# Kernel tuning notes

Measured on AMD Instinct MI355X. Metric: run time of the kernel, lower is better.

The kernel has to match this reference:

```python
import math
import jax, jax.numpy as jnp
import numpy as np

HEADS = 9
EMBED = 32
TEMPERATURE = 3000.0

def _conv1x1(x, W, b):
    # x: [B,C,H,W], W: [O,C], b: [O]  (1x1 conv == channel matmul)
    return jnp.einsum('bchw,oc->bohw', x, W) + b[None, :, None, None]

def setup_inputs() -> dict:
    key = jax.random.key(0)
    ks = jax.random.split(key, 14)
    B, H, W = 2, 64, 64
    h2, w2 = 32, 32
    hd = HEADS * EMBED  # 288
    s = 0.1
    return {
        'second_frame': jax.random.normal(ks[0], (B, 3, H, W), jnp.float32),
        'first_frame_aligned': jax.random.normal(ks[1], (B, 3, H, W), jnp.float32),
        'second_frame_feat': jax.random.normal(ks[2], (B, 4, h2, w2), jnp.float32),
        'first_frame_feat_aligned': jax.random.normal(ks[3], (B, 4, h2, w2), jnp.float32),
        'Wq': jax.random.normal(ks[4], (hd, 3), jnp.float32) * s,
        'bq': jax.random.normal(ks[5], (hd,), jnp.float32) * s,
        'Wk': jax.random.normal(ks[6], (hd, 3), jnp.float32) * s,
        'bk': jax.random.normal(ks[7], (hd,), jnp.float32) * s,
        'Wv': jax.random.normal(ks[8], (hd, 4), jnp.float32) * s,
        'bv': jax.random.normal(ks[9], (hd,), jnp.float32) * s,
        'Wp': jax.random.normal(ks[10], (4, hd), jnp.float32) * s,
        'bp': jax.random.normal(ks[11], (4,), jnp.float32) * s,
        'Wt': jax.random.normal(ks[12], (1, EMBED), jnp.float32) * s,
        'bt': jax.random.normal(ks[13], (1,), jnp.float32) * s,
    }

def reference(second_frame, first_frame_aligned, second_frame_feat,
              first_frame_feat_aligned, Wq, bq, Wk, bk, Wv, bv, Wp, bp, Wt, bt):
    B, _, H, W = second_frame.shape
    HW = H * W
    # bilinear upsample of aligned features to (H, W); half-pixel centers == align_corners=False
    feat_up = jax.image.resize(first_frame_feat_aligned,
                               (B, first_frame_feat_aligned.shape[1], H, W),
                               method='linear', antialias=False)
    Q = _conv1x1(second_frame, Wq, bq).reshape(B, HEADS, EMBED, HW)
    K = _conv1x1(first_frame_aligned, Wk, bk).reshape(B, HEADS, EMBED, HW)
    V = _conv1x1(feat_up, Wv, bv).reshape(B, HEADS, EMBED, HW)
    Qn = jnp.transpose(Q, (0, 1, 3, 2))                      # [B,h,HW,d]
    sim = jnp.einsum('bhnd,bhdm->bhnm', Qn, K) / math.sqrt(EMBED)  # [B,h,HW,HW]
    # learned per-query threshold from Q
    t = jnp.einsum('bhnd,od->bhno', Qn, Wt) + bt             # [B,h,HW,1]
    attn = jax.nn.relu((sim - t) / TEMPERATURE)              # no row normalization
    out = jnp.einsum('bhnm,bhdm->bhnd', attn, V)             # [B,h,HW,d]
    out = jnp.transpose(out, (0, 1, 3, 2)).reshape(B, HEADS * EMBED, H, W)
    out_feat = _conv1x1(out, Wp, bp)                         # [B,4,H,W]
    h2, w2 = second_frame_feat.shape[-2:]
    out_feat_down = jax.image.resize(out_feat, (B, out_feat.shape[1], h2, w2),
                                     method='linear', antialias=False)
    final_feat = second_frame_feat + out_feat_down
    return final_feat, out_feat_down
```

## Files before the change

### kernel.cpp

```cpp
#include <hip/hip_runtime.h>
#include <hip/hip_bf16.h>
#include <cstddef>

#define NHEADS 9
#define D 32
#define SQ 4096
#define ZSPLIT 8
#define MBLK (SQ / ZSPLIT)
#define CHUNKS (MBLK / 64)
#define KROW 40
#define VROW 72

typedef __attribute__((ext_vector_type(8))) short bf16x8;
typedef __attribute__((ext_vector_type(4))) short bf16x4;
typedef __attribute__((ext_vector_type(4))) float f32x4;

__device__ __forceinline__ unsigned int f2bf(float f) {
    unsigned int u = __float_as_uint(f);
    u += 0x7fffu + ((u >> 16) & 1u);
    return u >> 16;
}

__device__ __forceinline__ unsigned int trunc_pk(float lo, float hi) {
    return __builtin_amdgcn_perm(__float_as_uint(hi), __float_as_uint(lo),
                                 0x07060302u);
}

__device__ __forceinline__ bf16x8 relu_pack8(f32x4 s1, f32x4 s2) {
    const f32x4 zz = {0.f, 0.f, 0.f, 0.f};
    f32x4 a = __builtin_elementwise_max(s1, zz);
    f32x4 b = __builtin_elementwise_max(s2, zz);
    union { unsigned int u[4]; bf16x8 v; } P;
    P.u[0] = trunc_pk(a[0], a[1]);
    P.u[1] = trunc_pk(a[2], a[3]);
    P.u[2] = trunc_pk(b[0], b[1]);
    P.u[3] = trunc_pk(b[2], b[3]);
    return P.v;
}

__global__ __launch_bounds__(256) void prep_kernel(
    const float* __restrict__ x2, const float* __restrict__ x1,
    const float* __restrict__ feat1,
    const float* __restrict__ Wq, const float* __restrict__ bq,
    const float* __restrict__ Wk, const float* __restrict__ bk,
    const float* __restrict__ Wv, const float* __restrict__ bv,
    const float* __restrict__ Wt, const float* __restrict__ bt,
    unsigned short* __restrict__ Qb, unsigned short* __restrict__ Kb,
    unsigned short* __restrict__ Vt, float* __restrict__ tbuf,
    float* __restrict__ of)
{
    __shared__ unsigned short Vls[32 * 66];

    const int tid = threadIdx.x;
    int idx = blockIdx.x * blockDim.x + tid;
    if (idx < 2 * 4 * SQ) of[idx] = 0.0f;
    int g  = idx & 3;
    int nl = tid >> 2;
    int n  = (idx >> 2) & (SQ - 1);
    int bh = idx >> 14;
    int h  = bh % NHEADS;
    int b  = bh / NHEADS;

    float xs0 = x2[((size_t)b * 3 + 0) * SQ + n];
    float xs1 = x2[((size_t)b * 3 + 1) * SQ + n];
    float xs2 = x2[((size_t)b * 3 + 2) * SQ + n];
    float ys0 = x1[((size_t)b * 3 + 0) * SQ + n];
    float ys1 = x1[((size_t)b * 3 + 1) * SQ + n];
    float ys2 = x1[((size_t)b * 3 + 2) * SQ + n];

    int yy = n >> 6, xx = n & 63;
    int jy = yy >> 1, jx = xx >> 1;
    int j0, j1, i0, i1; float wy0, wy1, wx0, wx1;
    if (yy & 1) { j0 = jy; j1 = (jy < 31) ? jy + 1 : 31; wy0 = 0.75f; wy1 = 0.25f; }
    else        { j0 = (jy > 0) ? jy - 1 : 0; j1 = jy;   wy0 = 0.25f; wy1 = 0.75f; }
    if (xx & 1) { i0 = jx; i1 = (jx < 31) ? jx + 1 : 31; wx0 = 0.75f; wx1 = 0.25f; }
    else        { i0 = (jx > 0) ? jx - 1 : 0; i1 = jx;   wx0 = 0.25f; wx1 = 0.75f; }

    float fu[4];
#pragma unroll
    for (int c = 0; c < 4; ++c) {
        const float* f = feat1 + ((size_t)b * 4 + c) * 1024;
        fu[c] = wy0 * (wx0 * f[j0 * 32 + i0] + wx1 * f[j0 * 32 + i1]) +
                wy1 * (wx0 * f[j1 * 32 + i0] + wx1 * f[j1 * 32 + i1]);
    }

    const int d0 = g * 8;
    unsigned int qp[4], kp[4];
    float tpart = 0.0f;
#pragma unroll
    for (int j = 0; j < 8; ++j) {
        int d = d0 + j, hd = h * D + d;
        float q = bq[hd] + Wq[hd * 3] * xs0 + Wq[hd * 3 + 1] * xs1 + Wq[hd * 3 + 2] * xs2;
        float k = bk[hd] + Wk[hd * 3] * ys0 + Wk[hd * 3 + 1] * ys1 + Wk[hd * 3 + 2] * ys2;
        float v = bv[hd] + Wv[hd * 4] * fu[0] + Wv[hd * 4 + 1] * fu[1] +
                  Wv[hd * 4 + 2] * fu[2] + Wv[hd * 4 + 3] * fu[3];
        tpart += q * Wt[d];
        unsigned int qb_ = f2bf(q), kb_ = f2bf(k);
        if (j & 1) { qp[j >> 1] |= qb_ << 16; kp[j >> 1] |= kb_ << 16; }
        else       { qp[j >> 1]  = qb_;       kp[j >> 1]  = kb_; }
        Vls[d * 66 + nl] = (unsigned short)f2bf(v);
    }
    tpart += __shfl_xor(tpart, 1);
    tpart += __shfl_xor(tpart, 2);
    if (g == 0) tbuf[(size_t)bh * SQ + n] = tpart + bt[0];

    size_t base = ((size_t)bh * SQ + n) * D + d0;
    *(uint4*)(Qb + base) = make_uint4(qp[0], qp[1], qp[2], qp[3]);
    *(uint4*)(Kb + base) = make_uint4(kp[0], kp[1], kp[2], kp[3]);

    __syncthreads();
    {
        int r  = tid >> 3;
        int c4 = tid & 7;
        int n0 = (blockIdx.x & 63) * 64;
        unsigned int w0 = *(const unsigned int*)&Vls[r * 66 + c4 * 4];
        unsigned int w1 = *(const unsigned int*)&Vls[r * 66 + c4 * 4 + 2];
        *(uint2*)(Vt + ((size_t)bh * D + r) * SQ + n0 + c4 * 4) = make_uint2(w0, w1);
    }
}

__global__ __launch_bounds__(256, 4) void attn_kernel(
    const unsigned short* __restrict__ Qb,
    const unsigned short* __restrict__ Kb,
    const unsigned short* __restrict__ Vt,
    const float* __restrict__ tbuf,
    const float* __restrict__ Wp,
    float* __restrict__ of)
{
    __shared__ __align__(16) unsigned short Ks[64 * KROW];
    __shared__ __align__(16) unsigned short Vs[32 * VROW];

    const int bh   = blockIdx.y;
    const int h    = bh % NHEADS;
    const int b    = bh / NHEADS;
    const int n0   = blockIdx.x * 256;
    const int mc0  = blockIdx.z * MBLK;
    const int tid  = threadIdx.x;
    const int wave = tid >> 6;
    const int lane = tid & 63;
    const int l15  = lane & 15;
    const int quad = lane >> 4;

    const int nw = n0 + wave * 64;

    const unsigned short* qbase = Qb + ((size_t)bh * SQ + nw + l15) * D + quad * 8;
    bf16x8 qfA = *(const bf16x8*)(qbase);
    bf16x8 qfB = *(const bf16x8*)(qbase + 16 * D);
    bf16x8 qfC = *(const bf16x8*)(qbase + 32 * D);
    bf16x8 qfD = *(const bf16x8*)(qbase + 48 * D);

    const float SQRT32 = 5.656854249492381f;
    const float* tb = tbuf + (size_t)bh * SQ + nw + l15;
    float TA = tb[0]  * SQRT32;
    float TB = tb[16] * SQRT32;
    float TC = tb[32] * SQRT32;
    float TD = tb[48] * SQRT32;
    const f32x4 ciA = {-TA, -TA, -TA, -TA};
    const f32x4 ciB = {-TB, -TB, -TB, -TB};
    const f32x4 ciC = {-TC, -TC, -TC, -TC};
    const f32x4 ciD = {-TD, -TD, -TD, -TD};

    const uint4* Kg4 = (const uint4*)(Kb + (size_t)bh * SQ * D);
    const uint4* Vg4 = (const uint4*)(Vt + (size_t)bh * D * SQ);

    const int krow = tid >> 2;
    const int kcol = (tid & 3) * 8;
    const int kslot = (krow & 32) + 4 * ((krow >> 3) & 3) + (krow & 3) + ((krow & 4) << 2);
    unsigned short* kdst = Ks + kslot * KROW + kcol;
    const int vd = tid >> 3;
    const int vm = (tid & 7) * 8;
    unsigned short* vdst = Vs + vd * VROW + vm;
    const int vgbase = vd * (SQ / 8) + (mc0 >> 3) + (tid & 7);

    f32x4 accAl = {0.f,0.f,0.f,0.f}, accAh = {0.f,0.f,0.f,0.f};
    f32x4 accBl = {0.f,0.f,0.f,0.f}, accBh = {0.f,0.f,0.f,0.f};
    f32x4 accCl = {0.f,0.f,0.f,0.f}, accCh = {0.f,0.f,0.f,0.f};
    f32x4 accDl = {0.f,0.f,0.f,0.f}, accDh = {0.f,0.f,0.f,0.f};

    uint4 kreg = Kg4[(size_t)mc0 * 4 + tid];
    uint4 vreg = Vg4[vgbase];

    for (int c = 0; c < CHUNKS; ++c) {
        __syncthreads();
        *(uint4*)kdst = kreg;
        *(uint4*)vdst = vreg;
        kreg = Kg4[(size_t)(mc0 + (c + 1) * 64) * 4 + tid];
        vreg = Vg4[vgbase + (c + 1) * 8];
        __syncthreads();

#pragma unroll
        for (int g32 = 0; g32 < 2; ++g32) {
            const unsigned short* kbase = Ks + g32 * 32 * KROW;
            bf16x8 kf1 = *(const bf16x8*)(kbase + l15 * KROW + quad * 8);
            bf16x8 kf2 = *(const bf16x8*)(kbase + (16 + l15) * KROW + quad * 8);
            bf16x8 vlo = *(const bf16x8*)(Vs + l15 * VROW + g32 * 32 + quad * 8);
            bf16x8 vhi = *(const bf16x8*)(Vs + (l15 + 16) * VROW + g32 * 32 + quad * 8);

            f32x4 sA1 = __builtin_amdgcn_mfma_f32_16x16x32_bf16(kf1, qfA, ciA, 0, 0, 0);
            f32x4 sA2 = __builtin_amdgcn_mfma_f32_16x16x32_bf16(kf2, qfA, ciA, 0, 0, 0);
            f32x4 sB1 = __builtin_amdgcn_mfma_f32_16x16x32_bf16(kf1, qfB, ciB, 0, 0, 0);
            f32x4 sB2 = __builtin_amdgcn_mfma_f32_16x16x32_bf16(kf2, qfB, ciB, 0, 0, 0);
            f32x4 sC1 = __builtin_amdgcn_mfma_f32_16x16x32_bf16(kf1, qfC, ciC, 0, 0, 0);
            f32x4 sC2 = __builtin_amdgcn_mfma_f32_16x16x32_bf16(kf2, qfC, ciC, 0, 0, 0);
            f32x4 sD1 = __builtin_amdgcn_mfma_f32_16x16x32_bf16(kf1, qfD, ciD, 0, 0, 0);
            f32x4 sD2 = __builtin_amdgcn_mfma_f32_16x16x32_bf16(kf2, qfD, ciD, 0, 0, 0);

            bf16x8 pA = relu_pack8(sA1, sA2);
            bf16x8 pB = relu_pack8(sB1, sB2);
            bf16x8 pC = relu_pack8(sC1, sC2);
            bf16x8 pD = relu_pack8(sD1, sD2);

            accAl = __builtin_amdgcn_mfma_f32_16x16x32_bf16(vlo, pA, accAl, 0, 0, 0);
            accAh = __builtin_amdgcn_mfma_f32_16x16x32_bf16(vhi, pA, accAh, 0, 0, 0);
            accBl = __builtin_amdgcn_mfma_f32_16x16x32_bf16(vlo, pB, accBl, 0, 0, 0);
            accBh = __builtin_amdgcn_mfma_f32_16x16x32_bf16(vhi, pB, accBh, 0, 0, 0);
            accCl = __builtin_amdgcn_mfma_f32_16x16x32_bf16(vlo, pC, accCl, 0, 0, 0);
            accCh = __builtin_amdgcn_mfma_f32_16x16x32_bf16(vhi, pC, accCh, 0, 0, 0);
            accDl = __builtin_amdgcn_mfma_f32_16x16x32_bf16(vlo, pD, accDl, 0, 0, 0);
            accDh = __builtin_amdgcn_mfma_f32_16x16x32_bf16(vhi, pD, accDh, 0, 0, 0);
        }
    }

    const float s1 = 5.892556509887896e-05f;
    const float* wph = Wp + h * D + quad * 4;
#pragma unroll
    for (int o = 0; o < 4; ++o) {
        float cA = 0.f, cB = 0.f, cC = 0.f, cD = 0.f;
#pragma unroll
        for (int r = 0; r < 4; ++r) {
            float wlo = wph[o * 288 + r], whi = wph[o * 288 + 16 + r];
            cA += accAl[r] * wlo + accAh[r] * whi;
            cB += accBl[r] * wlo + accBh[r] * whi;
            cC += accCl[r] * wlo + accCh[r] * whi;
            cD += accDl[r] * wlo + accDh[r] * whi;
        }
        cA += __shfl_xor(cA, 16); cA += __shfl_xor(cA, 32);
        cB += __shfl_xor(cB, 16); cB += __shfl_xor(cB, 32);
        cC += __shfl_xor(cC, 16); cC += __shfl_xor(cC, 32);
        cD += __shfl_xor(cD, 16); cD += __shfl_xor(cD, 32);
        if (quad == 0) {
            float* ob = &of[((size_t)b * 4 + o) * SQ + nw + l15];
            atomicAdd(ob,      cA * s1);
            atomicAdd(ob + 16, cB * s1);
            atomicAdd(ob + 32, cC * s1);
            atomicAdd(ob + 48, cD * s1);
        }
    }
}

__global__ void final_kernel(const float* __restrict__ of,
                             const float* __restrict__ sff,
                             const float* __restrict__ bp,
                             float* __restrict__ dout)
{
    int tid = blockIdx.x * blockDim.x + threadIdx.x;
    if (tid >= 8192) return;
    int i  = tid & 31;
    int jj = (tid >> 5) & 31;
    int bo = tid >> 10;
    int o  = bo & 3;
    const float* src = of + (size_t)bo * SQ;
    int y = jj * 2, x = i * 2;
    float dval = 0.25f * (src[y * 64 + x] + src[y * 64 + x + 1] +
                          src[(y + 1) * 64 + x] + src[(y + 1) * 64 + x + 1]) + bp[o];
    dout[tid]        = sff[tid] + dval;
    dout[8192 + tid] = dval;
}

extern "C" void kernel_launch(void* const* d_in, const int* in_sizes, int n_in,
                              void* d_out, int out_size, void* d_ws, size_t ws_size,
                              hipStream_t stream)
{
    const float* second_frame = (const float*)d_in[0];
    const float* first_frame  = (const float*)d_in[1];
    const float* sff          = (const float*)d_in[2];
    const float* ffa          = (const float*)d_in[3];
    const float* Wq = (const float*)d_in[4];
    const float* bq = (const float*)d_in[5];
    const float* Wk = (const float*)d_in[6];
    const float* bk = (const float*)d_in[7];
    const float* Wv = (const float*)d_in[8];
    const float* bv = (const float*)d_in[9];
    const float* Wp = (const float*)d_in[10];
    const float* bp = (const float*)d_in[11];
    const float* Wt = (const float*)d_in[12];
    const float* bt = (const float*)d_in[13];
    float* out = (float*)d_out;

    char* ws = (char*)d_ws;
    const size_t QKV = (size_t)2 * NHEADS * SQ * D * sizeof(unsigned short);
    unsigned short* Qb = (unsigned short*)ws;
    unsigned short* Kb = (unsigned short*)(ws + QKV);
    unsigned short* Vt = (unsigned short*)(ws + 2 * QKV);
    float* tbuf = (float*)(ws + 3 * QKV);
    float* of   = (float*)(ws + 3 * QKV + (size_t)2 * NHEADS * SQ * sizeof(float));

    prep_kernel<<<1152, 256, 0, stream>>>(second_frame, first_frame, ffa,
                                          Wq, bq, Wk, bk, Wv, bv, Wt, bt,
                                          Qb, Kb, Vt, tbuf, of);
    dim3 ag(16, 18, ZSPLIT);
    attn_kernel<<<ag, 256, 0, stream>>>(Qb, Kb, Vt, tbuf, Wp, of);
    final_kernel<<<32, 256, 0, stream>>>(of, sff, bp, out);
}
```

Measured before the change: 136.7 us.

## Pre-tile K and V into MFMA fragment order and load directly from global

The prep kernel now writes K and V in 32-key tiles already permuted into the MFMA operand layout. This lets the attention kernel read its fragments straight from global memory (L2/L1) with register double-buffering instead of staging through LDS with two barriers per chunk. It removes the LDS traffic and synchronisation, but every wave now fetches the same K/V fragments independently from cache, and the prefetch on the last iteration reads one tile past the block's range.

```diff
diff --git a/kernel.cpp b/kernel.cpp
--- a/kernel.cpp
+++ b/kernel.cpp
@@ -7,12 +7,10 @@
 #define SQ 4096
 #define ZSPLIT 8
 #define MBLK (SQ / ZSPLIT)
-#define CHUNKS (MBLK / 64)
-#define KROW 40
-#define VROW 72
+#define NCH (MBLK / 32)
+#define NTILES (SQ / 32)
 
 typedef __attribute__((ext_vector_type(8))) short bf16x8;
-typedef __attribute__((ext_vector_type(4))) short bf16x4;
 typedef __attribute__((ext_vector_type(4))) float f32x4;
 
 __device__ __forceinline__ unsigned int f2bf(float f) {
@@ -45,7 +43,7 @@
     const float* __restrict__ Wk, const float* __restrict__ bk,
     const float* __restrict__ Wv, const float* __restrict__ bv,
     const float* __restrict__ Wt, const float* __restrict__ bt,
-    unsigned short* __restrict__ Qb, unsigned short* __restrict__ Kb,
+    unsigned short* __restrict__ Qb, unsigned short* __restrict__ Kt,
     unsigned short* __restrict__ Vt, float* __restrict__ tbuf,
     float* __restrict__ of)
 {
@@ -104,32 +102,40 @@
     tpart += __shfl_xor(tpart, 2);
     if (g == 0) tbuf[(size_t)bh * SQ + n] = tpart + bt[0];
 
-    size_t base = ((size_t)bh * SQ + n) * D + d0;
-    *(uint4*)(Qb + base) = make_uint4(qp[0], qp[1], qp[2], qp[3]);
-    *(uint4*)(Kb + base) = make_uint4(kp[0], kp[1], kp[2], kp[3]);
+    *(uint4*)(Qb + ((size_t)bh * SQ + n) * D + d0) = make_uint4(qp[0], qp[1], qp[2], qp[3]);
+
+    {
+        int chunk = n >> 5, w = n & 31;
+        int slot = ((w & 4) ? 16 : 0) + ((w >> 3) << 2) + (w & 3);
+        *(uint4*)(Kt + (((size_t)bh * NTILES + chunk) * 32 + slot) * 32 + d0) =
+            make_uint4(kp[0], kp[1], kp[2], kp[3]);
+    }
 
     __syncthreads();
     {
-        int r  = tid >> 3;
-        int c4 = tid & 7;
-        int n0 = (blockIdx.x & 63) * 64;
-        unsigned int w0 = *(const unsigned int*)&Vls[r * 66 + c4 * 4];
-        unsigned int w1 = *(const unsigned int*)&Vls[r * 66 + c4 * 4 + 2];
-        *(uint2*)(Vt + ((size_t)bh * D + r) * SQ + n0 + c4 * 4) = make_uint2(w0, w1);
+        int r    = tid >> 3;
+        int c8   = tid & 7;
+        int half = c8 >> 2;
+        int mloc = (c8 & 3) * 8;
+        int c0   = ((blockIdx.x & 63) * 64) >> 5;
+        const unsigned short* src = &Vls[r * 66 + half * 32 + mloc];
+        unsigned int w0 = *(const unsigned int*)(src);
+        unsigned int w1 = *(const unsigned int*)(src + 2);
+        unsigned int w2 = *(const unsigned int*)(src + 4);
+        unsigned int w3 = *(const unsigned int*)(src + 6);
+        *(uint4*)(Vt + (((size_t)bh * NTILES + c0 + half) * 32 + r) * 32 + mloc) =
+            make_uint4(w0, w1, w2, w3);
     }
 }
 
 __global__ __launch_bounds__(256, 4) void attn_kernel(
     const unsigned short* __restrict__ Qb,
-    const unsigned short* __restrict__ Kb,
+    const unsigned short* __restrict__ Kt,
     const unsigned short* __restrict__ Vt,
     const float* __restrict__ tbuf,
     const float* __restrict__ Wp,
     float* __restrict__ of)
 {
-    __shared__ __align__(16) unsigned short Ks[64 * KROW];
-    __shared__ __align__(16) unsigned short Vs[32 * VROW];
-
     const int bh   = blockIdx.y;
     const int h    = bh % NHEADS;
     const int b    = bh / NHEADS;
@@ -160,65 +166,52 @@
     const f32x4 ciC = {-TC, -TC, -TC, -TC};
     const f32x4 ciD = {-TD, -TD, -TD, -TD};
 
-    const uint4* Kg4 = (const uint4*)(Kb + (size_t)bh * SQ * D);
-    const uint4* Vg4 = (const uint4*)(Vt + (size_t)bh * D * SQ);
-
-    const int krow = tid >> 2;
-    const int kcol = (tid & 3) * 8;
-    const int kslot = (krow & 32) + 4 * ((krow >> 3) & 3) + (krow & 3) + ((krow & 4) << 2);
-    unsigned short* kdst = Ks + kslot * KROW + kcol;
-    const int vd = tid >> 3;
-    const int vm = (tid & 7) * 8;
-    unsigned short* vdst = Vs + vd * VROW + vm;
-    const int vgbase = vd * (SQ / 8) + (mc0 >> 3) + (tid & 7);
+    const int loff = l15 * 32 + quad * 8;
+    const unsigned short* kp = Kt + ((size_t)bh * NTILES + (mc0 >> 5)) * 1024 + loff;
+    const unsigned short* vp = Vt + ((size_t)bh * NTILES + (mc0 >> 5)) * 1024 + loff;
 
     f32x4 accAl = {0.f,0.f,0.f,0.f}, accAh = {0.f,0.f,0.f,0.f};
     f32x4 accBl = {0.f,0.f,0.f,0.f}, accBh = {0.f,0.f,0.f,0.f};
     f32x4 accCl = {0.f,0.f,0.f,0.f}, accCh = {0.f,0.f,0.f,0.f};
     f32x4 accDl = {0.f,0.f,0.f,0.f}, accDh = {0.f,0.f,0.f,0.f};
 
-    uint4 kreg = Kg4[(size_t)mc0 * 4 + tid];
-    uint4 vreg = Vg4[vgbase];
-
-    for (int c = 0; c < CHUNKS; ++c) {
-        __syncthreads();
-        *(uint4*)kdst = kreg;
-        *(uint4*)vdst = vreg;
-        kreg = Kg4[(size_t)(mc0 + (c + 1) * 64) * 4 + tid];
-        vreg = Vg4[vgbase + (c + 1) * 8];
-        __syncthreads();
-
-#pragma unroll
-        for (int g32 = 0; g32 < 2; ++g32) {
-            const unsigned short* kbase = Ks + g32 * 32 * KROW;
-            bf16x8 kf1 = *(const bf16x8*)(kbase + l15 * KROW + quad * 8);
-            bf16x8 kf2 = *(const bf16x8*)(kbase + (16 + l15) * KROW + quad * 8);
-            bf16x8 vlo = *(const bf16x8*)(Vs + l15 * VROW + g32 * 32 + quad * 8);
-            bf16x8 vhi = *(const bf16x8*)(Vs + (l15 + 16) * VROW + g32 * 32 + quad * 8);
-
-            f32x4 sA1 = __builtin_amdgcn_mfma_f32_16x16x32_bf16(kf1, qfA, ciA, 0, 0, 0);
-            f32x4 sA2 = __builtin_amdgcn_mfma_f32_16x16x32_bf16(kf2, qfA, ciA, 0, 0, 0);
-            f32x4 sB1 = __builtin_amdgcn_mfma_f32_16x16x32_bf16(kf1, qfB, ciB, 0, 0, 0);
-            f32x4 sB2 = __builtin_amdgcn_mfma_f32_16x16x32_bf16(kf2, qfB, ciB, 0, 0, 0);
-            f32x4 sC1 = __builtin_amdgcn_mfma_f32_16x16x32_bf16(kf1, qfC, ciC, 0, 0, 0);
-            f32x4 sC2 = __builtin_amdgcn_mfma_f32_16x16x32_bf16(kf2, qfC, ciC, 0, 0, 0);
-            f32x4 sD1 = __builtin_amdgcn_mfma_f32_16x16x32_bf16(kf1, qfD, ciD, 0, 0, 0);
-            f32x4 sD2 = __builtin_amdgcn_mfma_f32_16x16x32_bf16(kf2, qfD, ciD, 0, 0, 0);
-
-            bf16x8 pA = relu_pack8(sA1, sA2);
-            bf16x8 pB = relu_pack8(sB1, sB2);
-            bf16x8 pC = relu_pack8(sC1, sC2);
-            bf16x8 pD = relu_pack8(sD1, sD2);
-
-            accAl = __builtin_amdgcn_mfma_f32_16x16x32_bf16(vlo, pA, accAl, 0, 0, 0);
-            accAh = __builtin_amdgcn_mfma_f32_16x16x32_bf16(vhi, pA, accAh, 0, 0, 0);
-            accBl = __builtin_amdgcn_mfma_f32_16x16x32_bf16(vlo, pB, accBl, 0, 0, 0);
-            accBh = __builtin_amdgcn_mfma_f32_16x16x32_bf16(vhi, pB, accBh, 0, 0, 0);
-            accCl = __builtin_amdgcn_mfma_f32_16x16x32_bf16(vlo, pC, accCl, 0, 0, 0);
-            accCh = __builtin_amdgcn_mfma_f32_16x16x32_bf16(vhi, pC, accCh, 0, 0, 0);
-            accDl = __builtin_amdgcn_mfma_f32_16x16x32_bf16(vlo, pD, accDl, 0, 0, 0);
-            accDh = __builtin_amdgcn_mfma_f32_16x16x32_bf16(vhi, pD, accDh, 0, 0, 0);
-        }
+    bf16x8 kf1 = *(const bf16x8*)(kp);
+    bf16x8 kf2 = *(const bf16x8*)(kp + 512);
+    bf16x8 vlo = *(const bf16x8*)(vp);
+    bf16x8 vhi = *(const bf16x8*)(vp + 512);
+
+#pragma unroll 4
+    for (int it = 0; it < NCH; ++it) {
+        const size_t o = (size_t)(it + 1) * 1024;
+        bf16x8 kf1n = *(const bf16x8*)(kp + o);
+        bf16x8 kf2n = *(const bf16x8*)(kp + o + 512);
+        bf16x8 vlon = *(const bf16x8*)(vp + o);
+        bf16x8 vhin = *(const bf16x8*)(vp + o + 512);
+
+        f32x4 sA1 = __builtin_amdgcn_mfma_f32_16x16x32_bf16(kf1, qfA, ciA, 0, 0, 0);
+        f32x4 sA2 = __builtin_amdgcn_mfma_f32_16x16x32_bf16(kf2, qfA, ciA, 0, 0, 0);
+        f32x4 sB1 = __builtin_amdgcn_mfma_f32_16x16x32_bf16(kf1, qfB, ciB, 0, 0, 0);
+        f32x4 sB2 = __builtin_amdgcn_mfma_f32_16x16x32_bf16(kf2, qfB, ciB, 0, 0, 0);
+        f32x4 sC1 = __builtin_amdgcn_mfma_f32_16x16x32_bf16(kf1, qfC, ciC, 0, 0, 0);
+        f32x4 sC2 = __builtin_amdgcn_mfma_f32_16x16x32_bf16(kf2, qfC, ciC, 0, 0, 0);
+        f32x4 sD1 = __builtin_amdgcn_mfma_f32_16x16x32_bf16(kf1, qfD, ciD, 0, 0, 0);
+        f32x4 sD2 = __builtin_amdgcn_mfma_f32_16x16x32_bf16(kf2, qfD, ciD, 0, 0, 0);
+
+        bf16x8 pA = relu_pack8(sA1, sA2);
+        bf16x8 pB = relu_pack8(sB1, sB2);
+        bf16x8 pC = relu_pack8(sC1, sC2);
+        bf16x8 pD = relu_pack8(sD1, sD2);
+
+        accAl = __builtin_amdgcn_mfma_f32_16x16x32_bf16(vlo, pA, accAl, 0, 0, 0);
+        accAh = __builtin_amdgcn_mfma_f32_16x16x32_bf16(vhi, pA, accAh, 0, 0, 0);
+        accBl = __builtin_amdgcn_mfma_f32_16x16x32_bf16(vlo, pB, accBl, 0, 0, 0);
+        accBh = __builtin_amdgcn_mfma_f32_16x16x32_bf16(vhi, pB, accBh, 0, 0, 0);
+        accCl = __builtin_amdgcn_mfma_f32_16x16x32_bf16(vlo, pC, accCl, 0, 0, 0);
+        accCh = __builtin_amdgcn_mfma_f32_16x16x32_bf16(vhi, pC, accCh, 0, 0, 0);
+        accDl = __builtin_amdgcn_mfma_f32_16x16x32_bf16(vlo, pD, accDl, 0, 0, 0);
+        accDh = __builtin_amdgcn_mfma_f32_16x16x32_bf16(vhi, pD, accDh, 0, 0, 0);
+
+        kf1 = kf1n; kf2 = kf2n; vlo = vlon; vhi = vhin;
     }
 
     const float s1 = 5.892556509887896e-05f;
@@ -290,15 +283,15 @@
     char* ws = (char*)d_ws;
     const size_t QKV = (size_t)2 * NHEADS * SQ * D * sizeof(unsigned short);
     unsigned short* Qb = (unsigned short*)ws;
-    unsigned short* Kb = (unsigned short*)(ws + QKV);
+    unsigned short* Kt = (unsigned short*)(ws + QKV);
     unsigned short* Vt = (unsigned short*)(ws + 2 * QKV);
     float* tbuf = (float*)(ws + 3 * QKV);
     float* of   = (float*)(ws + 3 * QKV + (size_t)2 * NHEADS * SQ * sizeof(float));
 
     prep_kernel<<<1152, 256, 0, stream>>>(second_frame, first_frame, ffa,
                                           Wq, bq, Wk, bk, Wv, bv, Wt, bt,
-                                          Qb, Kb, Vt, tbuf, of);
+                                          Qb, Kt, Vt, tbuf, of);
     dim3 ag(16, 18, ZSPLIT);
-    attn_kernel<<<ag, 256, 0, stream>>>(Qb, Kb, Vt, tbuf, Wp, of);
+    attn_kernel<<<ag, 256, 0, stream>>>(Qb, Kt, Vt, tbuf, Wp, of);
     final_kernel<<<32, 256, 0, stream>>>(of, sff, bp, out);
 }
```

After: 145.0 us. +6.1%, slower.
